# Kernel tuning notes

Hardware: AMD Instinct MI355X
Metric: run time of the kernel (lower is better)

## Reference

```python
import jax, jax.numpy as jnp
import numpy as np

D_MODEL = 1024
NUM_HEADS = 16
HEAD_DIM = D_MODEL // NUM_HEADS
ROPE_THETA = 10000.0


def apply_rope(x, pos):
    # x: [B, H, S, Dh]; pos: [S] int. Interleaved-pair rotary embedding.
    d = x.shape[-1]
    inv_freq = 1.0 / (ROPE_THETA ** (jnp.arange(0, d, 2, dtype=jnp.float32) / d))  # [Dh/2]
    ang = pos.astype(jnp.float32)[:, None] * inv_freq[None, :]  # [S, Dh/2]
    cos, sin = jnp.cos(ang), jnp.sin(ang)
    x1 = x[..., 0::2]
    x2 = x[..., 1::2]
    r1 = x1 * cos - x2 * sin
    r2 = x1 * sin + x2 * cos
    return jnp.stack([r1, r2], axis=-1).reshape(x.shape)


def setup_inputs() -> dict:
    key = jax.random.key(0)
    ks = jax.random.split(key, 5)
    B, S = 4, 2048
    x = jax.random.normal(ks[0], (B, S, D_MODEL), dtype=jnp.float32)
    token_positions = jnp.arange(S, dtype=jnp.int32)
    scale = 1.0 / np.sqrt(D_MODEL)
    wq = jax.random.normal(ks[1], (D_MODEL, D_MODEL), dtype=jnp.float32) * scale
    wk = jax.random.normal(ks[2], (D_MODEL, D_MODEL), dtype=jnp.float32) * scale
    wv = jax.random.normal(ks[3], (D_MODEL, D_MODEL), dtype=jnp.float32) * scale
    wo = jax.random.normal(ks[4], (D_MODEL, D_MODEL), dtype=jnp.float32) * scale
    return {"x": x, "token_positions": token_positions, "wq": wq, "wk": wk, "wv": wv, "wo": wo}


def reference(x, token_positions, wq, wk, wv, wo):
    B, S, D = x.shape
    # Linear: einsum('d_out d_in, ... d_in -> ... d_out')
    def proj(w, t):
        return jnp.einsum('oi,bsi->bso', w, t)
    q = proj(wq, x).reshape(B, S, NUM_HEADS, HEAD_DIM).transpose(0, 2, 1, 3)  # [B,H,S,Dh]
    k = proj(wk, x).reshape(B, S, NUM_HEADS, HEAD_DIM).transpose(0, 2, 1, 3)
    v = proj(wv, x).reshape(B, S, NUM_HEADS, HEAD_DIM).transpose(0, 2, 1, 3)
    q = apply_rope(q, token_positions)
    k = apply_rope(k, token_positions)
    scores = jnp.einsum('bhqd,bhkd->bhqk', q, k) / jnp.sqrt(jnp.float32(HEAD_DIM))
    causal = jnp.tril(jnp.ones((S, S), dtype=bool))  # True = keep
    scores = jnp.where(causal, scores, -jnp.inf)
    attn = jax.nn.softmax(scores, axis=-1)
    out = jnp.einsum('bhqk,bhkd->bhqd', attn, v)  # [B,H,S,Dh]
    out = out.transpose(0, 2, 1, 3).reshape(B, S, D)
    return jnp.einsum('oi,bsi->bso', wo, out)
```

## Files before the change

### kernel.cpp

```cpp
#include <hip/hip_runtime.h>
#include <hip/hip_fp16.h>

#define DM   1024
#define NH   16
#define HD   64
#define BATCH 4
#define SEQ  2048
#define MROWS (BATCH*SEQ)
#define BHSD  ((size_t)BATCH*NH*SEQ*HD)

using f32x4 = __attribute__((ext_vector_type(4))) float;
using f16x8 = __attribute__((ext_vector_type(8))) _Float16;
using f16x4 = __attribute__((ext_vector_type(4))) _Float16;
using fp16x2 = __attribute__((ext_vector_type(2))) __fp16;
using u32x2 = __attribute__((ext_vector_type(2))) unsigned int;

__device__ __forceinline__ void gload_lds16(const void* g, void* l) {
    __builtin_amdgcn_global_load_lds(
        (const __attribute__((address_space(1))) void*)g,
        (__attribute__((address_space(3))) void*)l, 16, 0, 0);
}

__device__ __forceinline__ float red16_max(float v) {
    u32x2 r = __builtin_amdgcn_permlane16_swap(__float_as_uint(v), __float_as_uint(v), false, false);
    return fmaxf(__uint_as_float(r[0]), __uint_as_float(r[1]));
}
__device__ __forceinline__ float red32_max(float v) {
    u32x2 r = __builtin_amdgcn_permlane32_swap(__float_as_uint(v), __float_as_uint(v), false, false);
    return fmaxf(__uint_as_float(r[0]), __uint_as_float(r[1]));
}
__device__ __forceinline__ float red16_add(float v) {
    u32x2 r = __builtin_amdgcn_permlane16_swap(__float_as_uint(v), __float_as_uint(v), false, false);
    return __uint_as_float(r[0]) + __uint_as_float(r[1]);
}
__device__ __forceinline__ float red32_add(float v) {
    u32x2 r = __builtin_amdgcn_permlane32_swap(__float_as_uint(v), __float_as_uint(v), false, false);
    return __uint_as_float(r[0]) + __uint_as_float(r[1]);
}

__global__ __launch_bounds__(256) void f32_to_f16(const float* __restrict__ in,
                                                  _Float16* __restrict__ out, int n) {
    int i = (blockIdx.x * 256 + threadIdx.x) * 4;
    if (i >= n) return;
    float4 v = *(const float4*)(in + i);
    union { _Float16 h[4]; ushort4 u; } cv;
    cv.h[0] = (_Float16)v.x; cv.h[1] = (_Float16)v.y;
    cv.h[2] = (_Float16)v.z; cv.h[3] = (_Float16)v.w;
    *(ushort4*)(out + i) = cv.u;
}

__global__ __launch_bounds__(256) void rope_table(const int* __restrict__ pos,
                                                  float2* __restrict__ tab) {
    int idx = blockIdx.x * 256 + threadIdx.x;
    int s = idx >> 5, j = idx & 31;
    float p = (float)pos[s];
    float invf = powf(10000.0f, -(float)j / 32.0f);
    float ang = p * invf;
    tab[idx] = make_float2(cosf(ang), sinf(ang));
}

template<int MODE>
__global__ __launch_bounds__(512, 1)
void gemmP(const _Float16* __restrict__ A, const _Float16* __restrict__ Bw,
           float* __restrict__ outF, _Float16* __restrict__ qkv,
           const float2* __restrict__ rope) {
    constexpr int NK = DM / 32;
    constexpr int BN = MODE ? 256 : 128;
    constexpr int WTM = MODE ? 8 : 4;
    constexpr int BL = MODE ? 2 : 1;
    __shared__ __align__(16) _Float16 ldsA[3][256][32];
    __shared__ __align__(16) _Float16 ldsB[3][BN][32];

    const int tid  = threadIdx.x;
    const int lane = tid & 63;
    const int wid  = tid >> 6;

    const int nwg  = gridDim.x * gridDim.y;
    const int flat = blockIdx.y * gridDim.x + blockIdx.x;
    const int swz  = (flat % 8) * (nwg >> 3) + (flat >> 3);
    const int m0 = (swz % gridDim.x) * 256;
    const int n0 = (swz / gridDim.x) * BN;

    const int wm = MODE ? ((wid >> 2) * 128) : ((wid >> 1) * 64);
    const int wn = MODE ? ((wid & 3) * 64)   : ((wid & 1) * 64);
    const int g   = lane >> 4;
    const int r16 = lane & 15;

    const _Float16* srcA[2];
    int dstA[2];
    #pragma unroll
    for (int L = 0; L < 2; ++L) {
        const int u = L*512 + tid, row = u >> 2, c = (u & 3) ^ ((row >> 1) & 3);
        srcA[L] = A + (size_t)(m0 + row)*DM + c*8;
        dstA[L] = u*8;
    }
    const _Float16* srcB[BL];
    int dstB[BL];
    #pragma unroll
    for (int L = 0; L < BL; ++L) {
        const int u = L*512 + tid, row = u >> 2, c = (u & 3) ^ ((row >> 1) & 3);
        srcB[L] = Bw + (size_t)(n0 + row)*DM + c*8;
        dstB[L] = u*8;
    }

    #define STAGE(buf, kt) do {                                        \
        const int ko = (kt)*32;                                        \
        _Float16* bA = &ldsA[(buf)][0][0];                             \
        _Float16* bB = &ldsB[(buf)][0][0];                             \
        gload_lds16(srcA[0] + ko, bA + dstA[0]);                       \
        gload_lds16(srcA[1] + ko, bA + dstA[1]);                       \
        gload_lds16(srcB[0] + ko, bB + dstB[0]);                       \
        if constexpr (BL == 2) gload_lds16(srcB[1] + ko, bB + dstB[1]);\
    } while (0)

    f32x4 acc[WTM][4] = {};

    STAGE(0, 0);
    STAGE(1, 1);
    STAGE(2, 2);
    if constexpr (MODE == 1) asm volatile("s_waitcnt vmcnt(8)" ::: "memory");
    else                     asm volatile("s_waitcnt vmcnt(6)" ::: "memory");
    __builtin_amdgcn_s_barrier();

    int buf = 0;
    for (int t = 0; t < NK; ++t) {
        f16x8 af[WTM], bf[4];
        #pragma unroll
        for (int i = 0; i < WTM; ++i) {
            int row = wm + i*16 + r16;
            af[i] = *(const f16x8*)&ldsA[buf][row][(g ^ ((row >> 1) & 3)) * 8];
        }
        #pragma unroll
        for (int j = 0; j < 4; ++j) {
            int row = wn + j*16 + r16;
            bf[j] = *(const f16x8*)&ldsB[buf][row][(g ^ ((row >> 1) & 3)) * 8];
        }
        asm volatile("s_waitcnt lgkmcnt(0)" ::: "memory");
        __builtin_amdgcn_sched_barrier(0);
        __builtin_amdgcn_s_barrier();
        if (t + 3 < NK) STAGE(buf, t + 3);
        __builtin_amdgcn_s_setprio(1);
        #pragma unroll
        for (int i = 0; i < WTM; ++i)
            #pragma unroll
            for (int j = 0; j < 4; ++j)
                acc[i][j] = __builtin_amdgcn_mfma_f32_16x16x32_f16(af[i], bf[j], acc[i][j], 0, 0, 0);
        __builtin_amdgcn_s_setprio(0);
        if constexpr (MODE == 1) {
            if (t + 3 < NK)      asm volatile("s_waitcnt vmcnt(8)" ::: "memory");
            else if (t + 2 < NK) asm volatile("s_waitcnt vmcnt(4)" ::: "memory");
            else if (t + 1 < NK) asm volatile("s_waitcnt vmcnt(0)" ::: "memory");
        } else {
            if (t + 3 < NK)      asm volatile("s_waitcnt vmcnt(6)" ::: "memory");
            else if (t + 2 < NK) asm volatile("s_waitcnt vmcnt(3)" ::: "memory");
            else if (t + 1 < NK) asm volatile("s_waitcnt vmcnt(0)" ::: "memory");
        }
        __builtin_amdgcn_sched_barrier(0);
        __builtin_amdgcn_s_barrier();
        buf = (buf == 2) ? 0 : buf + 1;
    }
    #undef STAGE

    #pragma unroll
    for (int i = 0; i < WTM; ++i) {
        #pragma unroll
        for (int j = 0; j < 4; ++j) {
            if constexpr (MODE == 0) {
                #pragma unroll
                for (int r = 0; r < 4; ++r) {
                    const int m = m0 + wm + i*16 + g*4 + r;
                    const int n = n0 + wn + j*16 + r16;
                    outF[(size_t)m*DM + n] = acc[i][j][r];
                }
            } else {
                const int n = n0 + wn + j*16 + r16;
                const int sel = n >> 10;
                const int cc = n & 1023;
                const int h = cc >> 6, dd = cc & 63;
                if (sel == 2) {
                    const int mb = m0 + wm + i*16 + g*4;
                    const int s0 = mb & (SEQ - 1), b = mb >> 11;
                    f16x4 pk;
                    #pragma unroll
                    for (int r = 0; r < 4; ++r) pk[r] = (_Float16)acc[i][j][r];
                    *(f16x4*)(qkv + 2*BHSD + ((size_t)((b*NH + h)*HD + dd))*SEQ + s0) = pk;
                } else {
                    #pragma unroll
                    for (int r = 0; r < 4; ++r) {
                        const int m = m0 + wm + i*16 + g*4 + r;
                        float v = acc[i][j][r];
                        float vp = __shfl_xor(v, 1);
                        const int s = m & (SEQ - 1), b = m >> 11;
                        float2 cs = rope[(s << 5) + (dd >> 1)];
                        float o;
                        if (dd & 1) o = vp * cs.y + v * cs.x;
                        else        o = v * cs.x - vp * cs.y;
                        if (sel == 0) o *= 0.18033688f;
                        qkv[(size_t)sel*BHSD + ((size_t)((b*NH + h)*SEQ + s))*HD + dd] = (_Float16)o;
                    }
                }
            }
        }
    }
}

__device__ __forceinline__ void process_tile(
    const _Float16 (*__restrict__ Klb)[64], const _Float16 (*__restrict__ Vlb)[64],
    const f16x8 (&qf)[2], f32x4 (&ot)[4], float &m, float &l,
    const int Rq, const int kv0, const int g, const int r16) {

    f32x4 sT[4] = {};
    const int kchunkBase = r16 & 7;
    __builtin_amdgcn_s_setprio(1);
    #pragma unroll
    for (int ks = 0; ks < 2; ++ks) {
        #pragma unroll
        for (int n = 0; n < 4; ++n) {
            f16x8 kf = *(const f16x8*)&Klb[n*16 + r16][(((ks<<2)|g) ^ kchunkBase)*8];
            sT[n] = __builtin_amdgcn_mfma_f32_16x16x32_f16(kf, qf[ks], sT[n], 0, 0, 0);
        }
    }
    __builtin_amdgcn_s_setprio(0);

    const bool full = (kv0 + 63 <= Rq);
    float sv[16];
    if (full) {
        #pragma unroll
        for (int n = 0; n < 4; ++n)
            #pragma unroll
            for (int r = 0; r < 4; ++r) sv[n*4 + r] = sT[n][r];
    } else {
        const int q = Rq + r16;
        #pragma unroll
        for (int n = 0; n < 4; ++n)
            #pragma unroll
            for (int r = 0; r < 4; ++r)
                sv[n*4 + r] = (kv0 + n*16 + 4*g + r <= q) ? sT[n][r] : -INFINITY;
    }
    float mx = sv[0];
    #pragma unroll
    for (int i = 1; i < 16; ++i) mx = fmaxf(mx, sv[i]);
    mx = red32_max(red16_max(mx));
    const bool need = (mx > m + 8.f);
    if (__any(need)) {
        float mnew = need ? mx : m;
        float al = exp2f(m - mnew);
        m = mnew;
        l *= al;
        #pragma unroll
        for (int n = 0; n < 4; ++n) ot[n] *= al;
    }
    float ps = 0.f;
    #pragma unroll
    for (int i = 0; i < 16; ++i) { sv[i] = exp2f(sv[i] - m); ps += sv[i]; }
    l += red32_add(red16_add(ps));

    uint pk[4][2];
    #pragma unroll
    for (int t = 0; t < 4; ++t)
        #pragma unroll
        for (int rp = 0; rp < 2; ++rp) {
            union { fp16x2 h; uint u; } cv;
            cv.h = __builtin_amdgcn_cvt_pkrtz(sv[t*4 + 2*rp], sv[t*4 + 2*rp + 1]);
            pk[t][rp] = cv.u;
        }
    uint w[2][4];
    #pragma unroll
    for (int kk = 0; kk < 2; ++kk)
        #pragma unroll
        for (int rp = 0; rp < 2; ++rp) {
            u32x2 s32 = __builtin_amdgcn_permlane32_swap(pk[2*kk][rp], pk[2*kk + 1][rp], false, false);
            u32x2 s16 = __builtin_amdgcn_permlane16_swap(s32[0], s32[1], false, false);
            w[kk][rp]     = s16[0];
            w[kk][2 + rp] = s16[1];
        }

    __builtin_amdgcn_s_setprio(1);
    #pragma unroll
    for (int ks = 0; ks < 2; ++ks) {
        union { uint u[4]; f16x8 h; } pb;
        #pragma unroll
        for (int j2 = 0; j2 < 4; ++j2) pb.u[j2] = w[ks][j2];
        #pragma unroll
        for (int n = 0; n < 4; ++n) {
            f16x8 vf = *(const f16x8*)&Vlb[n*16 + r16][(((ks<<2)|g) ^ kchunkBase)*8];
            ot[n] = __builtin_amdgcn_mfma_f32_16x16x32_f16(vf, pb.h, ot[n], 0, 0, 0);
        }
    }
    __builtin_amdgcn_s_setprio(0);
}

__global__ __launch_bounds__(256, 4)
void attn_kernel(const _Float16* __restrict__ qkv, _Float16* __restrict__ ao) {
    const int tid = threadIdx.x, lane = tid & 63, w = tid >> 6;
    const int g = lane >> 4, r16 = lane & 15;
    const int bh = blockIdx.x;
    const int jq = blockIdx.y;
    const int q0h = (31 - jq) * 64, q0l = jq * 64;
    const _Float16* Q   = qkv + (size_t)bh * SEQ * HD;
    const _Float16* Kp  = qkv + BHSD + (size_t)bh * SEQ * HD;
    const _Float16* Vpt = qkv + 2*BHSD + (size_t)bh * SEQ * HD;

    __shared__ __align__(16) _Float16 Kl[2][64][64];
    __shared__ __align__(16) _Float16 Vl[2][64][64];

    const int rA = tid >> 3,        rB = 32 + (tid >> 3);
    const int lcA = (tid & 7) ^ (rA & 7), lcB = (tid & 7) ^ (rB & 7);
    const _Float16* KsrcA = Kp  + (size_t)rA*HD + lcA*8;
    const _Float16* KsrcB = Kp  + (size_t)rB*HD + lcB*8;
    const _Float16* VsrcA = Vpt + (size_t)rA*SEQ + lcA*8;
    const _Float16* VsrcB = Vpt + (size_t)rB*SEQ + lcB*8;

    const int Rh = q0h + w*16, Rl = q0l + w*16;
    f16x8 qfh[2], qfl[2];
    #pragma unroll
    for (int ks = 0; ks < 2; ++ks) {
        qfh[ks] = *(const f16x8*)(Q + (size_t)(Rh + r16)*HD + ks*32 + g*8);
        qfl[ks] = *(const f16x8*)(Q + (size_t)(Rl + r16)*HD + ks*32 + g*8);
    }

    f32x4 oth[4] = {}, otl[4] = {};
    float mh = -INFINITY, lh = 0.f, ml_ = -INFINITY, ll_ = 0.f;

    const int nth = (q0h >> 6) + 1;
    const int ntl = (q0l >> 6) + 1;

    #define STAGE(buf, kv0) do {                                              \
        gload_lds16(KsrcA + (size_t)(kv0)*HD, &Kl[(buf)][0][0] + tid*8);      \
        gload_lds16(KsrcB + (size_t)(kv0)*HD, &Kl[(buf)][0][0] + (256+tid)*8);\
        gload_lds16(VsrcA + (kv0),            &Vl[(buf)][0][0] + tid*8);      \
        gload_lds16(VsrcB + (kv0),            &Vl[(buf)][0][0] + (256+tid)*8);\
    } while (0)

    STAGE(0, 0);
    for (int kt = 0; kt < nth; ++kt) {
        const int kv0 = kt << 6;
        __syncthreads();
        if (kt + 1 < nth) STAGE((kt + 1) & 1, (kt + 1) << 6);
        const int buf = kt & 1;

        if (kv0 <= Rh + 15)
            process_tile(Kl[buf], Vl[buf], qfh, oth, mh, lh, Rh, kv0, g, r16);
        if (kt < ntl)
            process_tile(Kl[buf], Vl[buf], qfl, otl, ml_, ll_, Rl, kv0, g, r16);
    }
    #undef STAGE

    const int b = bh >> 4, h = bh & 15;
    const float invh = 1.0f / lh, invl = 1.0f / ll_;
    _Float16* dsth = ao + ((size_t)(b*SEQ + Rh + r16))*DM + h*HD + g*4;
    _Float16* dstl = ao + ((size_t)(b*SEQ + Rl + r16))*DM + h*HD + g*4;
    #pragma unroll
    for (int n = 0; n < 4; ++n) {
        f16x4 pkh, pkl;
        #pragma unroll
        for (int r = 0; r < 4; ++r) {
            pkh[r] = (_Float16)(oth[n][r] * invh);
            pkl[r] = (_Float16)(otl[n][r] * invl);
        }
        *(f16x4*)(dsth + n*16) = pkh;
        *(f16x4*)(dstl + n*16) = pkl;
    }
}

extern "C" void kernel_launch(void* const* d_in, const int* in_sizes, int n_in,
                              void* d_out, int out_size, void* d_ws, size_t ws_size,
                              hipStream_t stream) {
    const float* x  = (const float*)d_in[0];
    const int*   tp = (const int*)d_in[1];
    const float* wq = (const float*)d_in[2];
    const float* wk = (const float*)d_in[3];
    const float* wv = (const float*)d_in[4];
    const float* wo = (const float*)d_in[5];
    float* out = (float*)d_out;

    char* ws = (char*)d_ws;
    _Float16* xh  = (_Float16*)(ws);
    _Float16* whq = (_Float16*)(ws + 16777216);
    _Float16* woh = (_Float16*)(ws + 23068672);
    _Float16* qkv = (_Float16*)(ws + 25165824);
    _Float16* ao  = (_Float16*)(ws + 75497472);
    float2*   rope= (float2*)  (ws + 92274688);

    f32_to_f16<<<MROWS*DM/1024, 256, 0, stream>>>(x, xh, MROWS*DM);
    f32_to_f16<<<DM*DM/1024, 256, 0, stream>>>(wq, whq,            DM*DM);
    f32_to_f16<<<DM*DM/1024, 256, 0, stream>>>(wk, whq + DM*DM,    DM*DM);
    f32_to_f16<<<DM*DM/1024, 256, 0, stream>>>(wv, whq + 2*DM*DM,  DM*DM);
    f32_to_f16<<<DM*DM/1024, 256, 0, stream>>>(wo, woh,            DM*DM);
    rope_table<<<SEQ*32/256, 256, 0, stream>>>(tp, rope);

    gemmP<1><<<dim3(MROWS/256, 3*DM/256), 512, 0, stream>>>(xh, whq, nullptr, qkv, rope);
    attn_kernel<<<dim3(BATCH*NH, 16), 256, 0, stream>>>(qkv, ao);
    gemmP<0><<<dim3(MROWS/256, DM/128), 512, 0, stream>>>(ao, woh, out, nullptr, nullptr);
}
```

Measured before the change: 223.2 us.

## Restructure GEMM mainloop into 64-wide K tiles with split-half prefetch and new LDS swizzle

Replaces the triple-buffered 32-wide K loop in the projection GEMMs with a double-buffered loop over 64-wide K tiles, each split into two 32-wide halves. The next half-tile is issued into LDS while the current one is consumed. It also changes the LDS layout to pack row pairs into 64-element lines with an XOR swizzle, aiming to cut bank conflicts and barrier or waitcnt overhead per MFMA batch. The tighter prefetch distance and hand-tuned vmcnt values carry a risk of exposed load latency or synchronisation mistakes.

Result: no change. 219.9 us (-1.5%).

```diff
diff --git a/kernel.cpp b/kernel.cpp
--- a/kernel.cpp
+++ b/kernel.cpp
@@ -61,105 +61,105 @@
 
 template<int MODE>
 __global__ __launch_bounds__(512, 1)
-void gemmP(const _Float16* __restrict__ A, const _Float16* __restrict__ Bw,
+void gemmQ(const _Float16* __restrict__ A, const _Float16* __restrict__ Bw,
            float* __restrict__ outF, _Float16* __restrict__ qkv,
            const float2* __restrict__ rope) {
-    constexpr int NK = DM / 32;
-    constexpr int BN = MODE ? 256 : 128;
+    constexpr int NT  = DM / 64;
+    constexpr int BN  = MODE ? 256 : 128;
     constexpr int WTM = MODE ? 8 : 4;
-    constexpr int BL = MODE ? 2 : 1;
-    __shared__ __align__(16) _Float16 ldsA[3][256][32];
-    __shared__ __align__(16) _Float16 ldsB[3][BN][32];
-
-    const int tid  = threadIdx.x;
-    const int lane = tid & 63;
-    const int wid  = tid >> 6;
+    __shared__ __align__(16) _Float16 ldsA[2][2][256][32];
+    __shared__ __align__(16) _Float16 ldsB[2][2][BN][32];
+
+    const int tid = threadIdx.x, lane = tid & 63, wid = tid >> 6;
 
     const int nwg  = gridDim.x * gridDim.y;
     const int flat = blockIdx.y * gridDim.x + blockIdx.x;
-    const int swz  = (flat % 8) * (nwg >> 3) + (flat >> 3);
+    const int swz  = (flat & 7) * (nwg >> 3) + (flat >> 3);
     const int m0 = (swz % gridDim.x) * 256;
     const int n0 = (swz / gridDim.x) * BN;
 
     const int wm = MODE ? ((wid >> 2) * 128) : ((wid >> 1) * 64);
     const int wn = MODE ? ((wid & 3) * 64)   : ((wid & 1) * 64);
-    const int g   = lane >> 4;
-    const int r16 = lane & 15;
-
-    const _Float16* srcA[2];
-    int dstA[2];
+    const int g = lane >> 4, r16 = lane & 15;
+
+    const _Float16* sA[2]; int dA[2];
     #pragma unroll
     for (int L = 0; L < 2; ++L) {
-        const int u = L*512 + tid, row = u >> 2, c = (u & 3) ^ ((row >> 1) & 3);
-        srcA[L] = A + (size_t)(m0 + row)*DM + c*8;
-        dstA[L] = u*8;
-    }
-    const _Float16* srcB[BL];
-    int dstB[BL];
-    #pragma unroll
-    for (int L = 0; L < BL; ++L) {
-        const int u = L*512 + tid, row = u >> 2, c = (u & 3) ^ ((row >> 1) & 3);
-        srcB[L] = Bw + (size_t)(n0 + row)*DM + c*8;
-        dstB[L] = u*8;
-    }
-
-    #define STAGE(buf, kt) do {                                        \
-        const int ko = (kt)*32;                                        \
-        _Float16* bA = &ldsA[(buf)][0][0];                             \
-        _Float16* bB = &ldsB[(buf)][0][0];                             \
-        gload_lds16(srcA[0] + ko, bA + dstA[0]);                       \
-        gload_lds16(srcA[1] + ko, bA + dstA[1]);                       \
-        gload_lds16(srcB[0] + ko, bB + dstB[0]);                       \
-        if constexpr (BL == 2) gload_lds16(srcB[1] + ko, bB + dstB[1]);\
+        int u = L*512 + tid, sr = u >> 3, l = (u & 7) ^ (sr & 7);
+        sA[L] = A + (size_t)(m0 + sr*2 + (l >> 2))*DM + (l & 3)*8;
+        dA[L] = u*8;
+    }
+    const _Float16* sB[2]; int dB[2];
+    #pragma unroll
+    for (int L = 0; L < (MODE ? 2 : 1); ++L) {
+        int u = L*512 + tid, sr = u >> 3, l = (u & 7) ^ (sr & 7);
+        sB[L] = Bw + (size_t)(n0 + sr*2 + (l >> 2))*DM + (l & 3)*8;
+        dB[L] = u*8;
+    }
+
+    #define STG(buf, kh, kt) do {                                           \
+        const int ko = (kt)*64 + (kh)*32;                                   \
+        gload_lds16(sA[0] + ko, &ldsA[buf][kh][0][0] + dA[0]);              \
+        gload_lds16(sA[1] + ko, &ldsA[buf][kh][0][0] + dA[1]);              \
+        gload_lds16(sB[0] + ko, &ldsB[buf][kh][0][0] + dB[0]);              \
+        if constexpr (MODE == 1)                                            \
+            gload_lds16(sB[1] + ko, &ldsB[buf][kh][0][0] + dB[1]);          \
     } while (0)
 
+    const int rhalf = r16 >> 1;
+    const int tsw   = (((((r16 & 1) << 2) | g)) ^ rhalf) * 8;
+    const int laneA0 = ((wm >> 1) + rhalf) * 64 + tsw;
+    const int laneB0 = ((wn >> 1) + rhalf) * 64 + tsw;
+
     f32x4 acc[WTM][4] = {};
 
-    STAGE(0, 0);
-    STAGE(1, 1);
-    STAGE(2, 2);
-    if constexpr (MODE == 1) asm volatile("s_waitcnt vmcnt(8)" ::: "memory");
-    else                     asm volatile("s_waitcnt vmcnt(6)" ::: "memory");
+    STG(0, 0, 0);
+    STG(0, 1, 0);
+    STG(1, 0, 1);
+    if constexpr (MODE == 1) asm volatile("s_waitcnt vmcnt(4)" ::: "memory");
+    else                     asm volatile("s_waitcnt vmcnt(3)" ::: "memory");
+    __builtin_amdgcn_sched_barrier(0);
     __builtin_amdgcn_s_barrier();
 
-    int buf = 0;
-    for (int t = 0; t < NK; ++t) {
-        f16x8 af[WTM], bf[4];
-        #pragma unroll
-        for (int i = 0; i < WTM; ++i) {
-            int row = wm + i*16 + r16;
-            af[i] = *(const f16x8*)&ldsA[buf][row][(g ^ ((row >> 1) & 3)) * 8];
-        }
-        #pragma unroll
-        for (int j = 0; j < 4; ++j) {
-            int row = wn + j*16 + r16;
-            bf[j] = *(const f16x8*)&ldsB[buf][row][(g ^ ((row >> 1) & 3)) * 8];
-        }
-        asm volatile("s_waitcnt lgkmcnt(0)" ::: "memory");
-        __builtin_amdgcn_sched_barrier(0);
-        __builtin_amdgcn_s_barrier();
-        if (t + 3 < NK) STAGE(buf, t + 3);
-        __builtin_amdgcn_s_setprio(1);
-        #pragma unroll
-        for (int i = 0; i < WTM; ++i)
+    #pragma unroll 2
+    for (int t = 0; t < NT; ++t) {
+        const int cur = t & 1;
+        #pragma unroll
+        for (int ks = 0; ks < 2; ++ks) {
+            const _Float16* slA = &ldsA[cur][ks][0][0];
+            const _Float16* slB = &ldsB[cur][ks][0][0];
+            f16x8 af[WTM], bf[4];
+            #pragma unroll
+            for (int i = 0; i < WTM; ++i)
+                af[i] = *(const f16x8*)(slA + laneA0 + i*512);
             #pragma unroll
             for (int j = 0; j < 4; ++j)
-                acc[i][j] = __builtin_amdgcn_mfma_f32_16x16x32_f16(af[i], bf[j], acc[i][j], 0, 0, 0);
-        __builtin_amdgcn_s_setprio(0);
-        if constexpr (MODE == 1) {
-            if (t + 3 < NK)      asm volatile("s_waitcnt vmcnt(8)" ::: "memory");
-            else if (t + 2 < NK) asm volatile("s_waitcnt vmcnt(4)" ::: "memory");
-            else if (t + 1 < NK) asm volatile("s_waitcnt vmcnt(0)" ::: "memory");
-        } else {
-            if (t + 3 < NK)      asm volatile("s_waitcnt vmcnt(6)" ::: "memory");
-            else if (t + 2 < NK) asm volatile("s_waitcnt vmcnt(3)" ::: "memory");
-            else if (t + 1 < NK) asm volatile("s_waitcnt vmcnt(0)" ::: "memory");
-        }
-        __builtin_amdgcn_sched_barrier(0);
-        __builtin_amdgcn_s_barrier();
-        buf = (buf == 2) ? 0 : buf + 1;
-    }
-    #undef STAGE
+                bf[j] = *(const f16x8*)(slB + laneB0 + j*512);
+            if (ks == 0) { if (t + 1 < NT) STG(cur ^ 1, 1, t + 1); }
+            else         { if (t + 2 < NT) STG(cur,     0, t + 2); }
+            __builtin_amdgcn_s_barrier();
+            asm volatile("s_waitcnt lgkmcnt(0)" ::: "memory");
+            __builtin_amdgcn_sched_barrier(0);
+            __builtin_amdgcn_s_setprio(1);
+            #pragma unroll
+            for (int i = 0; i < WTM; ++i)
+                #pragma unroll
+                for (int j = 0; j < 4; ++j)
+                    acc[i][j] = __builtin_amdgcn_mfma_f32_16x16x32_f16(af[i], bf[j], acc[i][j], 0, 0, 0);
+            __builtin_amdgcn_s_setprio(0);
+            if (ks == 1 && t + 1 < NT) {
+                if (t + 2 < NT) {
+                    if constexpr (MODE == 1) asm volatile("s_waitcnt vmcnt(4)" ::: "memory");
+                    else                     asm volatile("s_waitcnt vmcnt(3)" ::: "memory");
+                } else {
+                    asm volatile("s_waitcnt vmcnt(0)" ::: "memory");
+                }
+                __builtin_amdgcn_sched_barrier(0);
+            }
+            __builtin_amdgcn_s_barrier();
+        }
+    }
+    #undef STG
 
     #pragma unroll
     for (int i = 0; i < WTM; ++i) {
@@ -389,7 +389,7 @@
     f32_to_f16<<<DM*DM/1024, 256, 0, stream>>>(wo, woh,            DM*DM);
     rope_table<<<SEQ*32/256, 256, 0, stream>>>(tp, rope);
 
-    gemmP<1><<<dim3(MROWS/256, 3*DM/256), 512, 0, stream>>>(xh, whq, nullptr, qkv, rope);
+    gemmQ<1><<<dim3(MROWS/256, 3*DM/256), 512, 0, stream>>>(xh, whq, nullptr, qkv, rope);
     attn_kernel<<<dim3(BATCH*NH, 16), 256, 0, stream>>>(qkv, ao);
-    gemmP<0><<<dim3(MROWS/256, DM/128), 512, 0, stream>>>(ao, woh, out, nullptr, nullptr);
-}
+    gemmQ<0><<<dim3(MROWS/256, DM/128), 512, 0, stream>>>(ao, woh, out, nullptr, nullptr);
+}
```
